# Optimization experiments

Measured on AMD Instinct MI355X. Metric: run time of the kernel, lower is better.

The kernel has to match this reference:

```python
import jax, jax.numpy as jnp
import numpy as np

C = 256
C8 = C // 8
B, H, W = 4, 64, 64


def setup_inputs() -> dict:
    key = jax.random.key(0)
    ks = jax.random.split(key, 10)
    s = lambda fan_in: 1.0 / np.sqrt(fan_in)
    return {
        "x": jax.random.normal(ks[0], (B, C, H, W), dtype=jnp.float32),
        "conv_w": jax.random.normal(ks[1], (C8, C), dtype=jnp.float32) * s(C),
        "conv_b": jax.random.normal(ks[2], (C8,), dtype=jnp.float32) * 0.01,
        "q_w": jax.random.normal(ks[3], (C8, C8), dtype=jnp.float32) * s(C8),
        "q_b": jax.random.normal(ks[4], (C8,), dtype=jnp.float32) * 0.01,
        "k_w": jax.random.normal(ks[5], (C8, C8), dtype=jnp.float32) * s(C8),
        "k_b": jax.random.normal(ks[6], (C8,), dtype=jnp.float32) * 0.01,
        "v_w": jax.random.normal(ks[7], (C, C8), dtype=jnp.float32) * s(C8),
        "v_b": jax.random.normal(ks[8], (C,), dtype=jnp.float32) * 0.01,
        "gamma": jax.random.normal(ks[9], (1,), dtype=jnp.float32) * 0.1,
    }


def reference(x, conv_w, conv_b, q_w, q_b, k_w, k_b, v_w, v_b, gamma):
    b, c, h, w = x.shape
    hw = h * w
    # 1x1 convs are channel-mixing matmuls over flattened spatial dims
    xf = x.reshape(b, c, hw)                                   # [B, C, HW]
    proj = jnp.einsum('dc,bcn->bdn', conv_w, xf) + conv_b[None, :, None]   # [B, C8, HW]
    q = jnp.einsum('ed,bdn->bne', q_w, proj) + q_b[None, None, :]          # [B, HW, C8]
    k = jnp.einsum('ed,bdn->ben', k_w, proj) + k_b[None, :, None]          # [B, C8, HW]
    v = jnp.einsum('cd,bdn->bcn', v_w, proj) + v_b[None, :, None]          # [B, C, HW]
    attn = jax.nn.softmax(jnp.einsum('bne,bem->bnm', q, k), axis=-1)       # [B, HW, HW]
    out = jnp.einsum('bcm,bnm->bcn', v, attn)                              # [B, C, HW]
    out = out.reshape(b, c, h, w)
    return gamma[0] * out + x
```

## Files before the change

### kernel.cpp

```cpp
#include <hip/hip_runtime.h>
#include <hip/hip_bf16.h>
#include <stdint.h>

#define B_   4
#define C_   256
#define C8_  32
#define HW_  4096
#define ROWS_ 320
#define MS_  4
#define L2E  1.4426950408889634f

typedef __attribute__((ext_vector_type(8)))  short  short8;
typedef __attribute__((ext_vector_type(8)))  ushort us8;
typedef __attribute__((ext_vector_type(2)))  float  f32x2;
typedef __attribute__((ext_vector_type(16))) float  f32x16;

#define WT_OFF    0
#define BALL_OFF  (256*320*4)
#define Q_OFF     (BALL_OFF + 1280)
#define KT_OFF    (Q_OFF  + B_*HW_*C8_*2)
#define V_OFF     (KT_OFF + B_*HW_*C8_*2)
#define PACC_OFF  (V_OFF  + B_*C_*HW_*2)
#define LPART_OFF (PACC_OFF + (size_t)MS_*B_*C_*HW_*2)

__device__ __forceinline__ ushort f2bf(float f) {
    union { float f; uint32_t u; } v; v.f = f;
    uint32_t u = v.u;
    uint32_t r = u + 0x7fffu + ((u >> 16) & 1u);
    return (ushort)(r >> 16);
}
__device__ __forceinline__ uint32_t pktr(float lo, float hi) {
    union { float f; uint32_t u; } a, b; a.f = lo; b.f = hi;
    return __builtin_amdgcn_perm(b.u, a.u, 0x07060302u);
}
__device__ __forceinline__ uint32_t pkrne(float lo, float hi) {
    uint32_t r;
    asm("v_cvt_pk_bf16_f32 %0, %1, %2" : "=v"(r) : "v"(lo), "v"(hi));
    return r;
}
__device__ __forceinline__ uint32_t fexp2_pk(float s0, float s1, f32x2& e01) {
    f32x2 s = {s0, s1};
    f32x2 y = __builtin_elementwise_fma(s, (f32x2)(8388608.0f),
                                        (f32x2)(1064992506.0f));
    y = __builtin_elementwise_max(y, (f32x2)(0.0f));
    union { int i; float f; } c0, c1;
    c0.i = (int)y.x;  c1.i = (int)y.y;
    e01.x = c0.f;  e01.y = c1.f;
    return __builtin_amdgcn_perm((uint32_t)c1.i, (uint32_t)c0.i, 0x07060302u);
}

__global__ __launch_bounds__(256) void k_setup(
    const float* __restrict__ conv_w, const float* __restrict__ conv_b,
    const float* __restrict__ q_w, const float* __restrict__ q_b,
    const float* __restrict__ k_w, const float* __restrict__ k_b,
    const float* __restrict__ v_w, const float* __restrict__ v_b,
    ushort* __restrict__ wbf, float* __restrict__ ball)
{
    int r = blockIdx.x;
    int c = threadIdx.x;
    const float* wrow;
    float bias;
    if (r < 32)       { wrow = q_w + r*32;      bias = q_b[r];      }
    else if (r < 64)  { wrow = k_w + (r-32)*32; bias = k_b[r-32];   }
    else              { wrow = v_w + (r-64)*32; bias = v_b[r-64];   }
    float acc = 0.f;
    #pragma unroll
    for (int d = 0; d < 32; ++d) acc += wrow[d] * conv_w[d*C_ + c];
    float scale = (r < 32) ? L2E : 1.0f;
    int lanew = (r & 31) + 32*((c >> 3) & 1);
    int fidx  = (c >> 4)*10 + (r >> 5);
    wbf[fidx*512 + lanew*8 + (c & 7)] = f2bf(acc * scale);
    if (c == 0) {
        float bb = bias;
        #pragma unroll
        for (int d = 0; d < 32; ++d) bb += wrow[d] * conv_b[d];
        ball[r] = bb * scale;
    }
}

__global__ __launch_bounds__(320) void k_qkv(
    const float* __restrict__ x, const ushort* __restrict__ wbf,
    const float* __restrict__ ball,
    ushort* __restrict__ qg, ushort* __restrict__ ktg, ushort* __restrict__ vg)
{
    __shared__ ushort tr[5][32*40];

    int blk = blockIdx.x;
    int b  = blk >> 7;
    int nt = blk & 127;
    int n0 = nt * 32;
    int t = threadIdx.x;
    int w = t >> 6, lane = t & 63;
    int l31 = lane & 31, h = lane >> 5;

    f32x16 acc[2];
    acc[0] = (f32x16)(0.f);
    acc[1] = (f32x16)(0.f);

    const float* xb = x + (size_t)b*C_*HW_ + n0 + l31;

    #pragma unroll 4
    for (int kc = 0; kc < 16; ++kc) {
        short8 a0 = *(const short8*)(wbf + (kc*10 + w*2    )*512 + lane*8);
        short8 a1 = *(const short8*)(wbf + (kc*10 + w*2 + 1)*512 + lane*8);
        const float* xc = xb + (size_t)(kc*16 + h*8)*HW_;
        float xv[8];
        #pragma unroll
        for (int j = 0; j < 8; ++j) xv[j] = xc[(size_t)j*HW_];
        union { uint32_t d[4]; short8 s8; } bf;
        #pragma unroll
        for (int j2 = 0; j2 < 4; ++j2) bf.d[j2] = pktr(xv[2*j2], xv[2*j2+1]);
        acc[0] = __builtin_amdgcn_mfma_f32_32x32x16_bf16(a0, bf.s8, acc[0], 0, 0, 0);
        acc[1] = __builtin_amdgcn_mfma_f32_32x32x16_bf16(a1, bf.s8, acc[1], 0, 0, 0);
    }

    #pragma unroll
    for (int mi = 0; mi < 2; ++mi) {
        int rowb = w*64 + mi*32;
        bool isQK = (rowb < 64);
        float4 bv[4];
        #pragma unroll
        for (int g = 0; g < 4; ++g)
            bv[g] = *(const float4*)(ball + rowb + g*8 + 4*h);
        if (isQK) {
            #pragma unroll
            for (int p = 0; p < 8; ++p) {
                int r0 = 2*p;
                int g  = r0 >> 2;
                int i0 = r0 & 3;
                float f0 = acc[mi][r0]     + ((const float*)&bv[g])[i0];
                float f1 = acc[mi][r0 + 1] + ((const float*)&bv[g])[i0 + 1];
                uint32_t pk = pkrne(f0, f1);
                int roff0 = i0 + 8*g + 4*h;
                *(uint32_t*)(&tr[w][l31*40 + roff0]) = pk;
            }
            #pragma unroll
            for (int f = 0; f < 2; ++f) {
                us8 frag = *(const us8*)(&tr[w][l31*40 + f*16 + h*8]);
                ushort* dstb = (rowb == 0) ? qg : ktg;
                size_t ad = ((size_t)((b*128 + nt)*2 + f) << 9) + lane*8;
                *(us8*)(dstb + ad) = frag;
            }
        } else {
            #pragma unroll
            for (int p = 0; p < 8; ++p) {
                int r0 = 2*p;
                int g  = r0 >> 2;
                int i0 = r0 & 3;
                float f0 = acc[mi][r0]     + ((const float*)&bv[g])[i0];
                float f1 = acc[mi][r0 + 1] + ((const float*)&bv[g])[i0 + 1];
                uint32_t pk = pkrne(f0, f1);
                int roff0 = i0 + 8*g + 4*h;
                tr[w][(roff0    )*40 + l31] = (ushort)pk;
                tr[w][(roff0 + 1)*40 + l31] = (ushort)(pk >> 16);
            }
            #pragma unroll
            for (int f = 0; f < 2; ++f) {
                us8 frag = *(const us8*)(&tr[w][l31*40 + f*16 + h*8]);
                int cblk = (rowb - 64) >> 5;
                int mb = nt*2 + f;
                size_t ad = ((size_t)((b*8 + cblk)*256 + mb) << 9) + lane*8;
                *(us8*)(vg + ad) = frag;
            }
        }
    }
}

__global__ __launch_bounds__(512, 4) void k_attn(
    const ushort* __restrict__ qg, const ushort* __restrict__ ktg,
    const ushort* __restrict__ vg,
    ushort* __restrict__ pacc, float* __restrict__ lpart)
{
    __shared__ ushort v_lds[2][16*512];
    __shared__ ushort kt_lds[2][4*512];

    int blk = blockIdx.x;
    int ms = blk & 3;
    int cs = (blk >> 2) & 1;
    int qb = (blk >> 3) & 15;
    int b  = blk >> 7;
    int t = threadIdx.x;
    int w = t >> 6, lane = t & 63;
    int l31 = lane & 31, h = lane >> 5;
    int mbase = ms*1024;

    short8 qf[2];
    #pragma unroll
    for (int ks = 0; ks < 2; ++ks)
        qf[ks] = *(const short8*)(qg
            + ((size_t)((b*128 + qb*8 + w)*2 + ks) << 9) + lane*8);

    f32x16 acc[4];
    #pragma unroll
    for (int j = 0; j < 4; ++j) acc[j] = (f32x16)(0.f);
    f32x2 lacc0 = {0.f, 0.f};
    f32x2 lacc1 = {0.f, 0.f};

    #define STAGE(buf, m0)                                                          \
    {                                                                               \
        _Pragma("unroll")                                                           \
        for (int ff = 0; ff < 2; ++ff) {                                            \
            int f = w*2 + ff;                                                       \
            int cfr = f >> 2, mf = f & 3;                                           \
            const ushort* src = vg + ((size_t)((b*8 + cs*4 + cfr)*256               \
                                 + ((m0) >> 4) + mf) << 9) + lane*8;                \
            __builtin_amdgcn_global_load_lds(                                       \
                (const __attribute__((address_space(1))) uint32_t*)src,             \
                (__attribute__((address_space(3))) uint32_t*)&v_lds[buf][f*512],    \
                16, 0, 0);                                                          \
        }                                                                           \
        if (w < 4) {                                                                \
            const ushort* src = ktg + ((size_t)((b*128 + ((m0) >> 5) + (w >> 1))*2  \
                                 + (w & 1)) << 9) + lane*8;                         \
            __builtin_amdgcn_global_load_lds(                                       \
                (const __attribute__((address_space(1))) uint32_t*)src,             \
                (__attribute__((address_space(3))) uint32_t*)&kt_lds[buf][w*512],   \
                16, 0, 0);                                                          \
        }                                                                           \
    }

    #define PMERGE(uu, lo8, hi8)                                                    \
    {                                                                               \
        union { uint32_t d[4]; short8 s8; } fe_, fo_;                               \
        auto r02 = __builtin_amdgcn_permlane32_swap((int)uu[0], (int)uu[2], false, false); \
        auto r13 = __builtin_amdgcn_permlane32_swap((int)uu[1], (int)uu[3], false, false); \
        auto r46 = __builtin_amdgcn_permlane32_swap((int)uu[4], (int)uu[6], false, false); \
        auto r57 = __builtin_amdgcn_permlane32_swap((int)uu[5], (int)uu[7], false, false); \
        fe_.d[0] = (uint32_t)r02[0];  fe_.d[1] = (uint32_t)r13[0];                  \
        fe_.d[2] = (uint32_t)r02[1];  fe_.d[3] = (uint32_t)r13[1];                  \
        fo_.d[0] = (uint32_t)r46[0];  fo_.d[1] = (uint32_t)r57[0];                  \
        fo_.d[2] = (uint32_t)r46[1];  fo_.d[3] = (uint32_t)r57[1];                  \
        lo8 = fe_.s8;  hi8 = fo_.s8;                                               \
    }

    STAGE(0, mbase)
    __syncthreads();

    int buf = 0;
    for (int it = 0; it < 16; ++it) {
        if (it + 1 < 16) STAGE(buf ^ 1, mbase + (it+1)*64)

        short8 kt0a = *(const short8*)(&kt_lds[buf][0*512 + lane*8]);
        short8 kt1a = *(const short8*)(&kt_lds[buf][1*512 + lane*8]);
        f32x16 s_a = (f32x16)(0.f);
        __builtin_amdgcn_s_setprio(1);
        s_a = __builtin_amdgcn_mfma_f32_32x32x16_bf16(kt0a, qf[0], s_a, 0, 0, 0);
        s_a = __builtin_amdgcn_mfma_f32_32x32x16_bf16(kt1a, qf[1], s_a, 0, 0, 0);
        __builtin_amdgcn_s_setprio(0);

        uint32_t ua[8];
        #pragma unroll
        for (int i = 0; i < 8; ++i) {
            f32x2 e01;
            ua[i] = fexp2_pk(s_a[2*i], s_a[2*i+1], e01);
            if (i & 1) lacc1 += e01; else lacc0 += e01;
        }
        short8 pfa0, pfa1;
        PMERGE(ua, pfa0, pfa1)

        short8 kt0b = *(const short8*)(&kt_lds[buf][2*512 + lane*8]);
        short8 kt1b = *(const short8*)(&kt_lds[buf][3*512 + lane*8]);
        f32x16 s_b = (f32x16)(0.f);
        s_b = __builtin_amdgcn_mfma_f32_32x32x16_bf16(kt0b, qf[0], s_b, 0, 0, 0);
        s_b = __builtin_amdgcn_mfma_f32_32x32x16_bf16(kt1b, qf[1], s_b, 0, 0, 0);

        uint32_t ub[8];
        #pragma unroll
        for (int i = 0; i < 8; ++i) {
            f32x2 e01;
            ub[i] = fexp2_pk(s_b[2*i], s_b[2*i+1], e01);
            if (i & 1) lacc1 += e01; else lacc0 += e01;
        }
        #pragma unroll
        for (int msub = 0; msub < 2; ++msub) {
            short8 pfm = msub ? pfa1 : pfa0;
            int ks16 = msub;
            #pragma unroll
            for (int cfr = 0; cfr < 4; ++cfr) {
                short8 vf = *(const short8*)(&v_lds[buf][(cfr*4 + ks16)*512 + lane*8]);
                acc[cfr] = __builtin_amdgcn_mfma_f32_32x32x16_bf16(vf, pfm, acc[cfr], 0, 0, 0);
            }
        }
        short8 pfb0, pfb1;
        PMERGE(ub, pfb0, pfb1)

        __builtin_amdgcn_s_setprio(1);
        #pragma unroll
        for (int msub = 0; msub < 2; ++msub) {
            short8 pfm = msub ? pfb1 : pfb0;
            int ks16 = 2 + msub;
            #pragma unroll
            for (int cfr = 0; cfr < 4; ++cfr) {
                short8 vf = *(const short8*)(&v_lds[buf][(cfr*4 + ks16)*512 + lane*8]);
                acc[cfr] = __builtin_amdgcn_mfma_f32_32x32x16_bf16(vf, pfm, acc[cfr], 0, 0, 0);
            }
        }
        __builtin_amdgcn_s_setprio(0);

        __syncthreads();
        buf ^= 1;
    }

    f32x2 lacc = lacc0 + lacc1;
    float lsum = lacc.x + lacc.y;
    {
        union { float f; int i; } cv; cv.f = lsum;
        cv.i = __shfl_xor(cv.i, 32);
        lsum += cv.f;
    }
    if (cs == 0 && h == 0)
        lpart[(size_t)(ms*B_ + b)*HW_ + qb*256 + w*32 + l31] = lsum;

    int blkl = ((ms*B_ + b)*16 + qb)*2 + cs;
    #pragma unroll
    for (int cfr = 0; cfr < 4; ++cfr) {
        union { uint32_t d[8]; us8 hlf[2]; } pk;
        #pragma unroll
        for (int i = 0; i < 8; ++i)
            pk.d[i] = pktr(acc[cfr][2*i], acc[cfr][2*i+1]);
        ushort* dst = pacc + ((size_t)(blkl*32 + w*4 + cfr) << 10);
        *(us8*)(dst + lane*8)       = pk.hlf[0];
        *(us8*)(dst + 512 + lane*8) = pk.hlf[1];
    }
    #undef STAGE
    #undef PMERGE
}

__global__ __launch_bounds__(256) void k_comb(
    const ushort* __restrict__ pacc, const float* __restrict__ lpart,
    const float* __restrict__ x, const float* __restrict__ gamma_p,
    float* __restrict__ out)
{
    __shared__ float lds_acc[128*36];

    int blk = blockIdx.x;
    int w  = blk & 7;
    int cs = (blk >> 3) & 1;
    int qb = (blk >> 4) & 15;
    int b  = blk >> 8;
    int t = threadIdx.x;

    int l31 = t & 31;
    int h   = (t >> 5) & 1;
    int cfr = (t >> 6) & 3;
    int q = qb*256 + w*32 + l31;
    int lanef = h*32 + l31;

    float sum[16];
    #pragma unroll
    for (int k = 0; k < 16; ++k) sum[k] = 0.f;
    float lt = 0.f;

    #pragma unroll
    for (int ms = 0; ms < MS_; ++ms) {
        int blkl = ((ms*B_ + b)*16 + qb)*2 + cs;
        const ushort* pp = pacc + ((size_t)(blkl*32 + w*4 + cfr) << 10) + lanef*8;
        us8 a0 = *(const us8*)pp;
        us8 a1 = *(const us8*)(pp + 512);
        #pragma unroll
        for (int k = 0; k < 8; ++k) {
            union { uint32_t u; float f; } cv;
            cv.u = ((uint32_t)a0[k]) << 16;  sum[k]   += cv.f;
            cv.u = ((uint32_t)a1[k]) << 16;  sum[k+8] += cv.f;
        }
        lt += lpart[(size_t)(ms*B_ + b)*HW_ + q];
    }

    float rl = gamma_p[0] / lt;
    #pragma unroll
    for (int k = 0; k < 16; ++k) {
        int c = cfr*32 + (k & 3) + 8*(k >> 2) + 4*h;
        lds_acc[c*36 + l31] = sum[k]*rl;
    }
    __syncthreads();

    const float* xb = x + ((size_t)(b*C_ + cs*128))*HW_ + qb*256 + w*32;
    float* ob = out + ((size_t)(b*C_ + cs*128))*HW_ + qb*256 + w*32;
    #pragma unroll
    for (int i = 0; i < 4; ++i) {
        int s = t + i*256;
        int c = s >> 3, qg = s & 7;
        float4 a = *(const float4*)(&lds_acc[c*36 + qg*4]);
        size_t off = (size_t)c*HW_ + qg*4;
        float4 xv = *(const float4*)(xb + off);
        a.x += xv.x; a.y += xv.y; a.z += xv.z; a.w += xv.w;
        *(float4*)(ob + off) = a;
    }
}

extern "C" void kernel_launch(void* const* d_in, const int* in_sizes, int n_in,
                              void* d_out, int out_size, void* d_ws, size_t ws_size,
                              hipStream_t stream)
{
    const float* x      = (const float*)d_in[0];
    const float* conv_w = (const float*)d_in[1];
    const float* conv_b = (const float*)d_in[2];
    const float* q_w    = (const float*)d_in[3];
    const float* q_b    = (const float*)d_in[4];
    const float* k_w    = (const float*)d_in[5];
    const float* k_b    = (const float*)d_in[6];
    const float* v_w    = (const float*)d_in[7];
    const float* v_b    = (const float*)d_in[8];
    const float* gamma  = (const float*)d_in[9];
    float* out = (float*)d_out;

    char* ws = (char*)d_ws;
    ushort* wbf   = (ushort*)(ws + WT_OFF);
    float*  ball  = (float*)(ws + BALL_OFF);
    ushort* qg    = (ushort*)(ws + Q_OFF);
    ushort* ktg   = (ushort*)(ws + KT_OFF);
    ushort* vg    = (ushort*)(ws + V_OFF);
    ushort* pacc  = (ushort*)(ws + PACC_OFF);
    float*  lpart = (float*)(ws + LPART_OFF);

    k_setup<<<ROWS_, 256, 0, stream>>>(conv_w, conv_b, q_w, q_b, k_w, k_b,
                                       v_w, v_b, wbf, ball);
    k_qkv<<<B_*128, 320, 0, stream>>>(x, wbf, ball, qg, ktg, vg);
    k_attn<<<512, 512, 0, stream>>>(qg, ktg, vg, pacc, lpart);
    k_comb<<<1024, 256, 0, stream>>>(pacc, lpart, x, gamma, out);
}
```

Measured before the change: 154.3 us.

## Triple-buffer K/V LDS staging with explicit vmcnt waits in attention loop

Grows the V and K^T LDS staging from two buffers to three, so tiles are prefetched two iterations ahead instead of one. Each iteration now begins with a partial s_waitcnt vmcnt that leaves the newest stage in flight, followed by a single raw s_barrier. This replaces the __syncthreads that waited on all outstanding loads at the end of each iteration. The goal is to hide more global-to-LDS latency behind the MFMA and exp work. The cost is 50% more LDS per block, which could limit how many blocks fit on a CU. The correctness of the hand-written vmcnt counts depends on each wave's exact load count.

Measured after the change: 154.8 us. No clear change (+0.4%).

```diff
diff --git a/kernel.cpp b/kernel.cpp
--- a/kernel.cpp
+++ b/kernel.cpp
@@ -171,8 +171,8 @@
     const ushort* __restrict__ vg,
     ushort* __restrict__ pacc, float* __restrict__ lpart)
 {
-    __shared__ ushort v_lds[2][16*512];
-    __shared__ ushort kt_lds[2][4*512];
+    __shared__ ushort v_lds[3][16*512];
+    __shared__ ushort kt_lds[3][4*512];
 
     int blk = blockIdx.x;
     int ms = blk & 3;
@@ -196,7 +196,7 @@
     f32x2 lacc0 = {0.f, 0.f};
     f32x2 lacc1 = {0.f, 0.f};
 
-    #define STAGE(buf, m0)                                                          \
+    #define STAGE(bi, m0)                                                           \
     {                                                                               \
         _Pragma("unroll")                                                           \
         for (int ff = 0; ff < 2; ++ff) {                                            \
@@ -206,7 +206,7 @@
                                  + ((m0) >> 4) + mf) << 9) + lane*8;                \
             __builtin_amdgcn_global_load_lds(                                       \
                 (const __attribute__((address_space(1))) uint32_t*)src,             \
-                (__attribute__((address_space(3))) uint32_t*)&v_lds[buf][f*512],    \
+                (__attribute__((address_space(3))) uint32_t*)&v_lds[bi][f*512],     \
                 16, 0, 0);                                                          \
         }                                                                           \
         if (w < 4) {                                                                \
@@ -214,7 +214,7 @@
                                  + (w & 1)) << 9) + lane*8;                         \
             __builtin_amdgcn_global_load_lds(                                       \
                 (const __attribute__((address_space(1))) uint32_t*)src,             \
-                (__attribute__((address_space(3))) uint32_t*)&kt_lds[buf][w*512],   \
+                (__attribute__((address_space(3))) uint32_t*)&kt_lds[bi][w*512],    \
                 16, 0, 0);                                                          \
         }                                                                           \
     }
@@ -234,14 +234,25 @@
     }
 
     STAGE(0, mbase)
-    __syncthreads();
-
-    int buf = 0;
+    STAGE(1, mbase + 64)
+
+    int b0 = 0, b1 = 1, b2 = 2;
+    #pragma unroll 1
     for (int it = 0; it < 16; ++it) {
-        if (it + 1 < 16) STAGE(buf ^ 1, mbase + (it+1)*64)
-
-        short8 kt0a = *(const short8*)(&kt_lds[buf][0*512 + lane*8]);
-        short8 kt1a = *(const short8*)(&kt_lds[buf][1*512 + lane*8]);
+        if (it == 15)   { asm volatile("s_waitcnt vmcnt(0)" ::: "memory"); }
+        else if (w < 4) { asm volatile("s_waitcnt vmcnt(3)" ::: "memory"); }
+        else            { asm volatile("s_waitcnt vmcnt(2)" ::: "memory"); }
+        __builtin_amdgcn_s_barrier();
+        __builtin_amdgcn_sched_barrier(0);
+
+        if (it + 2 < 16) STAGE(b2, mbase + (it+2)*64)
+        __builtin_amdgcn_sched_barrier(0);
+
+        const ushort* vbuf = &v_lds[b0][0];
+        const ushort* kbuf = &kt_lds[b0][0];
+
+        short8 kt0a = *(const short8*)(kbuf + 0*512 + lane*8);
+        short8 kt1a = *(const short8*)(kbuf + 1*512 + lane*8);
         f32x16 s_a = (f32x16)(0.f);
         __builtin_amdgcn_s_setprio(1);
         s_a = __builtin_amdgcn_mfma_f32_32x32x16_bf16(kt0a, qf[0], s_a, 0, 0, 0);
@@ -258,8 +269,8 @@
         short8 pfa0, pfa1;
         PMERGE(ua, pfa0, pfa1)
 
-        short8 kt0b = *(const short8*)(&kt_lds[buf][2*512 + lane*8]);
-        short8 kt1b = *(const short8*)(&kt_lds[buf][3*512 + lane*8]);
+        short8 kt0b = *(const short8*)(kbuf + 2*512 + lane*8);
+        short8 kt1b = *(const short8*)(kbuf + 3*512 + lane*8);
         f32x16 s_b = (f32x16)(0.f);
         s_b = __builtin_amdgcn_mfma_f32_32x32x16_bf16(kt0b, qf[0], s_b, 0, 0, 0);
         s_b = __builtin_amdgcn_mfma_f32_32x32x16_bf16(kt1b, qf[1], s_b, 0, 0, 0);
@@ -277,7 +288,7 @@
             int ks16 = msub;
             #pragma unroll
             for (int cfr = 0; cfr < 4; ++cfr) {
-                short8 vf = *(const short8*)(&v_lds[buf][(cfr*4 + ks16)*512 + lane*8]);
+                short8 vf = *(const short8*)(vbuf + (cfr*4 + ks16)*512 + lane*8);
                 acc[cfr] = __builtin_amdgcn_mfma_f32_32x32x16_bf16(vf, pfm, acc[cfr], 0, 0, 0);
             }
         }
@@ -291,14 +302,13 @@
             int ks16 = 2 + msub;
             #pragma unroll
             for (int cfr = 0; cfr < 4; ++cfr) {
-                short8 vf = *(const short8*)(&v_lds[buf][(cfr*4 + ks16)*512 + lane*8]);
+                short8 vf = *(const short8*)(vbuf + (cfr*4 + ks16)*512 + lane*8);
                 acc[cfr] = __builtin_amdgcn_mfma_f32_32x32x16_bf16(vf, pfm, acc[cfr], 0, 0, 0);
             }
         }
         __builtin_amdgcn_s_setprio(0);
 
-        __syncthreads();
-        buf ^= 1;
+        int tb = b0; b0 = b1; b1 = b2; b2 = tb;
     }
 
     f32x2 lacc = lacc0 + lacc1;
```

## Fuse four kernels into one persistent kernel with software grid barriers

Applied to the files above, without the earlier changes.

Merges the setup, QKV projection, attention and combine kernels into a single 512-block kernel separated by atomic-counter grid barriers, and adds a memset to reset the barrier counters. The aim is to remove three kernel launch gaps and their tail effects. In exchange, all 512 blocks must be co-resident for the barrier to work, and the QKV phase leaves 192 threads per block idle. Barrier spin cost and reduced occupancy flexibility may offset the launch savings.

New measurement: 344.8 us. +123.5%, slower.

```diff
diff --git a/kernel.cpp b/kernel.cpp
--- a/kernel.cpp
+++ b/kernel.cpp
@@ -8,6 +8,7 @@
 #define HW_  4096
 #define ROWS_ 320
 #define MS_  4
+#define NB_  512
 #define L2E  1.4426950408889634f
 
 typedef __attribute__((ext_vector_type(8)))  short  short8;
@@ -22,6 +23,7 @@
 #define V_OFF     (KT_OFF + B_*HW_*C8_*2)
 #define PACC_OFF  (V_OFF  + B_*C_*HW_*2)
 #define LPART_OFF (PACC_OFF + (size_t)MS_*B_*C_*HW_*2)
+#define GB_OFF    (LPART_OFF + (size_t)MS_*B_*HW_*4)
 
 __device__ __forceinline__ ushort f2bf(float f) {
     union { float f; uint32_t u; } v; v.f = f;
@@ -49,342 +51,375 @@
     return __builtin_amdgcn_perm((uint32_t)c1.i, (uint32_t)c0.i, 0x07060302u);
 }
 
-__global__ __launch_bounds__(256) void k_setup(
+__device__ __forceinline__ void gridbar(uint32_t* cnt, uint32_t* gen) {
+    __syncthreads();
+    if (threadIdx.x == 0) {
+        __threadfence();
+        uint32_t g = __hip_atomic_load(gen, __ATOMIC_RELAXED,
+                                       __HIP_MEMORY_SCOPE_AGENT);
+        uint32_t old = __hip_atomic_fetch_add(cnt, 1u, __ATOMIC_ACQ_REL,
+                                              __HIP_MEMORY_SCOPE_AGENT);
+        if (old == NB_ - 1u) {
+            __hip_atomic_store(cnt, 0u, __ATOMIC_RELAXED,
+                               __HIP_MEMORY_SCOPE_AGENT);
+            __hip_atomic_fetch_add(gen, 1u, __ATOMIC_RELEASE,
+                                   __HIP_MEMORY_SCOPE_AGENT);
+        } else {
+            long tmo = 200000000;
+            while (__hip_atomic_load(gen, __ATOMIC_RELAXED,
+                                     __HIP_MEMORY_SCOPE_AGENT) == g
+                   && --tmo > 0) ;
+        }
+        __threadfence();
+    }
+    __syncthreads();
+}
+
+__global__ __launch_bounds__(512, 4) void k_fused(
+    const float* __restrict__ x,
     const float* __restrict__ conv_w, const float* __restrict__ conv_b,
     const float* __restrict__ q_w, const float* __restrict__ q_b,
     const float* __restrict__ k_w, const float* __restrict__ k_b,
     const float* __restrict__ v_w, const float* __restrict__ v_b,
-    ushort* __restrict__ wbf, float* __restrict__ ball)
+    const float* __restrict__ gamma_p,
+    float* __restrict__ out,
+    ushort* __restrict__ wbf, float* __restrict__ ball,
+    ushort* __restrict__ qg, ushort* __restrict__ ktg, ushort* __restrict__ vg,
+    ushort* __restrict__ pacc, float* __restrict__ lpart,
+    uint32_t* __restrict__ gb)
 {
-    int r = blockIdx.x;
-    int c = threadIdx.x;
-    const float* wrow;
-    float bias;
-    if (r < 32)       { wrow = q_w + r*32;      bias = q_b[r];      }
-    else if (r < 64)  { wrow = k_w + (r-32)*32; bias = k_b[r-32];   }
-    else              { wrow = v_w + (r-64)*32; bias = v_b[r-64];   }
-    float acc = 0.f;
-    #pragma unroll
-    for (int d = 0; d < 32; ++d) acc += wrow[d] * conv_w[d*C_ + c];
-    float scale = (r < 32) ? L2E : 1.0f;
-    int lanew = (r & 31) + 32*((c >> 3) & 1);
-    int fidx  = (c >> 4)*10 + (r >> 5);
-    wbf[fidx*512 + lanew*8 + (c & 7)] = f2bf(acc * scale);
-    if (c == 0) {
-        float bb = bias;
-        #pragma unroll
-        for (int d = 0; d < 32; ++d) bb += wrow[d] * conv_b[d];
-        ball[r] = bb * scale;
+    __shared__ __align__(16) char smem[40960];
+
+    int blk = blockIdx.x;
+    int t = threadIdx.x;
+    uint32_t* gb_cnt = gb;
+    uint32_t* gb_gen = gb + 1;
+
+    if (blk < ROWS_ && t < 256) {
+        int r = blk;
+        int c = t;
+        const float* wrow;
+        float bias;
+        if (r < 32)       { wrow = q_w + r*32;      bias = q_b[r];      }
+        else if (r < 64)  { wrow = k_w + (r-32)*32; bias = k_b[r-32];   }
+        else              { wrow = v_w + (r-64)*32; bias = v_b[r-64];   }
+        float acc = 0.f;
+        #pragma unroll
+        for (int d = 0; d < 32; ++d) acc += wrow[d] * conv_w[d*C_ + c];
+        float scale = (r < 32) ? L2E : 1.0f;
+        int lanew = (r & 31) + 32*((c >> 3) & 1);
+        int fidx  = (c >> 4)*10 + (r >> 5);
+        wbf[fidx*512 + lanew*8 + (c & 7)] = f2bf(acc * scale);
+        if (c == 0) {
+            float bb = bias;
+            #pragma unroll
+            for (int d = 0; d < 32; ++d) bb += wrow[d] * conv_b[d];
+            ball[r] = bb * scale;
+        }
     }
-}
-
-__global__ __launch_bounds__(320) void k_qkv(
-    const float* __restrict__ x, const ushort* __restrict__ wbf,
-    const float* __restrict__ ball,
-    ushort* __restrict__ qg, ushort* __restrict__ ktg, ushort* __restrict__ vg)
-{
-    __shared__ ushort tr[5][32*40];
-
-    int blk = blockIdx.x;
-    int b  = blk >> 7;
-    int nt = blk & 127;
-    int n0 = nt * 32;
-    int t = threadIdx.x;
-    int w = t >> 6, lane = t & 63;
-    int l31 = lane & 31, h = lane >> 5;
-
-    f32x16 acc[2];
-    acc[0] = (f32x16)(0.f);
-    acc[1] = (f32x16)(0.f);
-
-    const float* xb = x + (size_t)b*C_*HW_ + n0 + l31;
-
-    #pragma unroll 4
-    for (int kc = 0; kc < 16; ++kc) {
-        short8 a0 = *(const short8*)(wbf + (kc*10 + w*2    )*512 + lane*8);
-        short8 a1 = *(const short8*)(wbf + (kc*10 + w*2 + 1)*512 + lane*8);
-        const float* xc = xb + (size_t)(kc*16 + h*8)*HW_;
-        float xv[8];
-        #pragma unroll
-        for (int j = 0; j < 8; ++j) xv[j] = xc[(size_t)j*HW_];
-        union { uint32_t d[4]; short8 s8; } bf;
-        #pragma unroll
-        for (int j2 = 0; j2 < 4; ++j2) bf.d[j2] = pktr(xv[2*j2], xv[2*j2+1]);
-        acc[0] = __builtin_amdgcn_mfma_f32_32x32x16_bf16(a0, bf.s8, acc[0], 0, 0, 0);
-        acc[1] = __builtin_amdgcn_mfma_f32_32x32x16_bf16(a1, bf.s8, acc[1], 0, 0, 0);
+    gridbar(gb_cnt, gb_gen);
+
+    if (t < 320) {
+        ushort (*tr)[32*40] = (ushort (*)[32*40])smem;
+
+        int b  = blk >> 7;
+        int nt = blk & 127;
+        int n0 = nt * 32;
+        int w = t >> 6, lane = t & 63;
+        int l31 = lane & 31, h = lane >> 5;
+
+        f32x16 acc[2];
+        acc[0] = (f32x16)(0.f);
+        acc[1] = (f32x16)(0.f);
+
+        const float* xb = x + (size_t)b*C_*HW_ + n0 + l31;
+
+        #pragma unroll 4
+        for (int kc = 0; kc < 16; ++kc) {
+            short8 a0 = *(const short8*)(wbf + (kc*10 + w*2    )*512 + lane*8);
+            short8 a1 = *(const short8*)(wbf + (kc*10 + w*2 + 1)*512 + lane*8);
+            const float* xc = xb + (size_t)(kc*16 + h*8)*HW_;
+            float xv[8];
+            #pragma unroll
+            for (int j = 0; j < 8; ++j) xv[j] = xc[(size_t)j*HW_];
+            union { uint32_t d[4]; short8 s8; } bf;
+            #pragma unroll
+            for (int j2 = 0; j2 < 4; ++j2) bf.d[j2] = pktr(xv[2*j2], xv[2*j2+1]);
+            acc[0] = __builtin_amdgcn_mfma_f32_32x32x16_bf16(a0, bf.s8, acc[0], 0, 0, 0);
+            acc[1] = __builtin_amdgcn_mfma_f32_32x32x16_bf16(a1, bf.s8, acc[1], 0, 0, 0);
+        }
+
+        #pragma unroll
+        for (int mi = 0; mi < 2; ++mi) {
+            int rowb = w*64 + mi*32;
+            bool isQK = (rowb < 64);
+            float4 bv[4];
+            #pragma unroll
+            for (int g = 0; g < 4; ++g)
+                bv[g] = *(const float4*)(ball + rowb + g*8 + 4*h);
+            if (isQK) {
+                #pragma unroll
+                for (int p = 0; p < 8; ++p) {
+                    int r0 = 2*p;
+                    int g  = r0 >> 2;
+                    int i0 = r0 & 3;
+                    float f0 = acc[mi][r0]     + ((const float*)&bv[g])[i0];
+                    float f1 = acc[mi][r0 + 1] + ((const float*)&bv[g])[i0 + 1];
+                    uint32_t pk = pkrne(f0, f1);
+                    int roff0 = i0 + 8*g + 4*h;
+                    *(uint32_t*)(&tr[w][l31*40 + roff0]) = pk;
+                }
+                #pragma unroll
+                for (int f = 0; f < 2; ++f) {
+                    us8 frag = *(const us8*)(&tr[w][l31*40 + f*16 + h*8]);
+                    ushort* dstb = (rowb == 0) ? qg : ktg;
+                    size_t ad = ((size_t)((b*128 + nt)*2 + f) << 9) + lane*8;
+                    *(us8*)(dstb + ad) = frag;
+                }
+            } else {
+                #pragma unroll
+                for (int p = 0; p < 8; ++p) {
+                    int r0 = 2*p;
+                    int g  = r0 >> 2;
+                    int i0 = r0 & 3;
+                    float f0 = acc[mi][r0]     + ((const float*)&bv[g])[i0];
+                    float f1 = acc[mi][r0 + 1] + ((const float*)&bv[g])[i0 + 1];
+                    uint32_t pk = pkrne(f0, f1);
+                    int roff0 = i0 + 8*g + 4*h;
+                    tr[w][(roff0    )*40 + l31] = (ushort)pk;
+                    tr[w][(roff0 + 1)*40 + l31] = (ushort)(pk >> 16);
+                }
+                #pragma unroll
+                for (int f = 0; f < 2; ++f) {
+                    us8 frag = *(const us8*)(&tr[w][l31*40 + f*16 + h*8]);
+                    int cblk = (rowb - 64) >> 5;
+                    int mb = nt*2 + f;
+                    size_t ad = ((size_t)((b*8 + cblk)*256 + mb) << 9) + lane*8;
+                    *(us8*)(vg + ad) = frag;
+                }
+            }
+        }
     }
-
-    #pragma unroll
-    for (int mi = 0; mi < 2; ++mi) {
-        int rowb = w*64 + mi*32;
-        bool isQK = (rowb < 64);
-        float4 bv[4];
-        #pragma unroll
-        for (int g = 0; g < 4; ++g)
-            bv[g] = *(const float4*)(ball + rowb + g*8 + 4*h);
-        if (isQK) {
-            #pragma unroll
-            for (int p = 0; p < 8; ++p) {
-                int r0 = 2*p;
-                int g  = r0 >> 2;
-                int i0 = r0 & 3;
-                float f0 = acc[mi][r0]     + ((const float*)&bv[g])[i0];
-                float f1 = acc[mi][r0 + 1] + ((const float*)&bv[g])[i0 + 1];
-                uint32_t pk = pkrne(f0, f1);
-                int roff0 = i0 + 8*g + 4*h;
-                *(uint32_t*)(&tr[w][l31*40 + roff0]) = pk;
-            }
-            #pragma unroll
-            for (int f = 0; f < 2; ++f) {
-                us8 frag = *(const us8*)(&tr[w][l31*40 + f*16 + h*8]);
-                ushort* dstb = (rowb == 0) ? qg : ktg;
-                size_t ad = ((size_t)((b*128 + nt)*2 + f) << 9) + lane*8;
-                *(us8*)(dstb + ad) = frag;
-            }
-        } else {
-            #pragma unroll
-            for (int p = 0; p < 8; ++p) {
-                int r0 = 2*p;
-                int g  = r0 >> 2;
-                int i0 = r0 & 3;
-                float f0 = acc[mi][r0]     + ((const float*)&bv[g])[i0];
-                float f1 = acc[mi][r0 + 1] + ((const float*)&bv[g])[i0 + 1];
-                uint32_t pk = pkrne(f0, f1);
-                int roff0 = i0 + 8*g + 4*h;
-                tr[w][(roff0    )*40 + l31] = (ushort)pk;
-                tr[w][(roff0 + 1)*40 + l31] = (ushort)(pk >> 16);
-            }
-            #pragma unroll
-            for (int f = 0; f < 2; ++f) {
-                us8 frag = *(const us8*)(&tr[w][l31*40 + f*16 + h*8]);
-                int cblk = (rowb - 64) >> 5;
-                int mb = nt*2 + f;
-                size_t ad = ((size_t)((b*8 + cblk)*256 + mb) << 9) + lane*8;
-                *(us8*)(vg + ad) = frag;
-            }
-        }
+    gridbar(gb_cnt, gb_gen);
+
+    {
+        ushort* v_lds  = (ushort*)smem;
+        ushort* kt_lds = (ushort*)(smem + 32768);
+
+        int ms = blk & 3;
+        int cs = (blk >> 2) & 1;
+        int qb = (blk >> 3) & 15;
+        int b  = blk >> 7;
+        int w = t >> 6, lane = t & 63;
+        int l31 = lane & 31, h = lane >> 5;
+        int mbase = ms*1024;
+
+        short8 qf[2];
+        #pragma unroll
+        for (int ks = 0; ks < 2; ++ks)
+            qf[ks] = *(const short8*)(qg
+                + ((size_t)((b*128 + qb*8 + w)*2 + ks) << 9) + lane*8);
+
+        f32x16 acc[4];
+        #pragma unroll
+        for (int j = 0; j < 4; ++j) acc[j] = (f32x16)(0.f);
+        f32x2 lacc0 = {0.f, 0.f};
+        f32x2 lacc1 = {0.f, 0.f};
+
+        #define STAGE(bi, m0)                                                          \
+        {                                                                              \
+            _Pragma("unroll")                                                          \
+            for (int ff = 0; ff < 2; ++ff) {                                           \
+                int f = w*2 + ff;                                                      \
+                int cfr = f >> 2, mf = f & 3;                                          \
+                const ushort* src = vg + ((size_t)((b*8 + cs*4 + cfr)*256              \
+                                     + ((m0) >> 4) + mf) << 9) + lane*8;               \
+                __builtin_amdgcn_global_load_lds(                                      \
+                    (const __attribute__((address_space(1))) uint32_t*)src,            \
+                    (__attribute__((address_space(3))) uint32_t*)                      \
+                        &v_lds[(bi)*8192 + f*512],                                     \
+                    16, 0, 0);                                                         \
+            }                                                                          \
+            if (w < 4) {                                                               \
+                const ushort* src = ktg + ((size_t)((b*128 + ((m0) >> 5) + (w >> 1))*2 \
+                                     + (w & 1)) << 9) + lane*8;                        \
+                __builtin_amdgcn_global_load_lds(                                      \
+                    (const __attribute__((address_space(1))) uint32_t*)src,            \
+                    (__attribute__((address_space(3))) uint32_t*)                      \
+                        &kt_lds[(bi)*2048 + w*512],                                    \
+                    16, 0, 0);                                                         \
+            }                                                                          \
+        }
+
+        #define PMERGE(uu, lo8, hi8)                                                   \
+        {                                                                              \
+            union { uint32_t d[4]; short8 s8; } fe_, fo_;                              \
+            auto r02 = __builtin_amdgcn_permlane32_swap((int)uu[0], (int)uu[2], false, false); \
+            auto r13 = __builtin_amdgcn_permlane32_swap((int)uu[1], (int)uu[3], false, false); \
+            auto r46 = __builtin_amdgcn_permlane32_swap((int)uu[4], (int)uu[6], false, false); \
+            auto r57 = __builtin_amdgcn_permlane32_swap((int)uu[5], (int)uu[7], false, false); \
+            fe_.d[0] = (uint32_t)r02[0];  fe_.d[1] = (uint32_t)r13[0];                 \
+            fe_.d[2] = (uint32_t)r02[1];  fe_.d[3] = (uint32_t)r13[1];                 \
+            fo_.d[0] = (uint32_t)r46[0];  fo_.d[1] = (uint32_t)r57[0];                 \
+            fo_.d[2] = (uint32_t)r46[1];  fo_.d[3] = (uint32_t)r57[1];                 \
+            lo8 = fe_.s8;  hi8 = fo_.s8;                                              \
+        }
+
+        STAGE(0, mbase)
+        __syncthreads();
+
+        int buf = 0;
+        for (int it = 0; it < 16; ++it) {
+            if (it + 1 < 16) STAGE(buf ^ 1, mbase + (it+1)*64)
+
+            const ushort* vbuf = &v_lds[buf*8192];
+            const ushort* kbuf = &kt_lds[buf*2048];
+
+            short8 kt0a = *(const short8*)(kbuf + 0*512 + lane*8);
+            short8 kt1a = *(const short8*)(kbuf + 1*512 + lane*8);
+            f32x16 s_a = (f32x16)(0.f);
+            __builtin_amdgcn_s_setprio(1);
+            s_a = __builtin_amdgcn_mfma_f32_32x32x16_bf16(kt0a, qf[0], s_a, 0, 0, 0);
+            s_a = __builtin_amdgcn_mfma_f32_32x32x16_bf16(kt1a, qf[1], s_a, 0, 0, 0);
+            __builtin_amdgcn_s_setprio(0);
+
+            uint32_t ua[8];
+            #pragma unroll
+            for (int i = 0; i < 8; ++i) {
+                f32x2 e01;
+                ua[i] = fexp2_pk(s_a[2*i], s_a[2*i+1], e01);
+                if (i & 1) lacc1 += e01; else lacc0 += e01;
+            }
+            short8 pfa0, pfa1;
+            PMERGE(ua, pfa0, pfa1)
+
+            short8 kt0b = *(const short8*)(kbuf + 2*512 + lane*8);
+            short8 kt1b = *(const short8*)(kbuf + 3*512 + lane*8);
+            f32x16 s_b = (f32x16)(0.f);
+            s_b = __builtin_amdgcn_mfma_f32_32x32x16_bf16(kt0b, qf[0], s_b, 0, 0, 0);
+            s_b = __builtin_amdgcn_mfma_f32_32x32x16_bf16(kt1b, qf[1], s_b, 0, 0, 0);
+
+            uint32_t ub[8];
+            #pragma unroll
+            for (int i = 0; i < 8; ++i) {
+                f32x2 e01;
+                ub[i] = fexp2_pk(s_b[2*i], s_b[2*i+1], e01);
+                if (i & 1) lacc1 += e01; else lacc0 += e01;
+            }
+            #pragma unroll
+            for (int msub = 0; msub < 2; ++msub) {
+                short8 pfm = msub ? pfa1 : pfa0;
+                int ks16 = msub;
+                #pragma unroll
+                for (int cfr = 0; cfr < 4; ++cfr) {
+                    short8 vf = *(const short8*)(vbuf + (cfr*4 + ks16)*512 + lane*8);
+                    acc[cfr] = __builtin_amdgcn_mfma_f32_32x32x16_bf16(vf, pfm, acc[cfr], 0, 0, 0);
+                }
+            }
+            short8 pfb0, pfb1;
+            PMERGE(ub, pfb0, pfb1)
+
+            __builtin_amdgcn_s_setprio(1);
+            #pragma unroll
+            for (int msub = 0; msub < 2; ++msub) {
+                short8 pfm = msub ? pfb1 : pfb0;
+                int ks16 = 2 + msub;
+                #pragma unroll
+                for (int cfr = 0; cfr < 4; ++cfr) {
+                    short8 vf = *(const short8*)(vbuf + (cfr*4 + ks16)*512 + lane*8);
+                    acc[cfr] = __builtin_amdgcn_mfma_f32_32x32x16_bf16(vf, pfm, acc[cfr], 0, 0, 0);
+                }
+            }
+            __builtin_amdgcn_s_setprio(0);
+
+            __syncthreads();
+            buf ^= 1;
+        }
+
+        f32x2 lacc = lacc0 + lacc1;
+        float lsum = lacc.x + lacc.y;
+        {
+            union { float f; int i; } cv; cv.f = lsum;
+            cv.i = __shfl_xor(cv.i, 32);
+            lsum += cv.f;
+        }
+        if (cs == 0 && h == 0)
+            lpart[(size_t)(ms*B_ + b)*HW_ + qb*256 + w*32 + l31] = lsum;
+
+        int blkl = ((ms*B_ + b)*16 + qb)*2 + cs;
+        #pragma unroll
+        for (int cfr = 0; cfr < 4; ++cfr) {
+            union { uint32_t d[8]; us8 hlf[2]; } pk;
+            #pragma unroll
+            for (int i = 0; i < 8; ++i)
+                pk.d[i] = pktr(acc[cfr][2*i], acc[cfr][2*i+1]);
+            ushort* dst = pacc + ((size_t)(blkl*32 + w*4 + cfr) << 10);
+            *(us8*)(dst + lane*8)       = pk.hlf[0];
+            *(us8*)(dst + 512 + lane*8) = pk.hlf[1];
+        }
+        #undef STAGE
+        #undef PMERGE
     }
-}
-
-__global__ __launch_bounds__(512, 4) void k_attn(
-    const ushort* __restrict__ qg, const ushort* __restrict__ ktg,
-    const ushort* __restrict__ vg,
-    ushort* __restrict__ pacc, float* __restrict__ lpart)
-{
-    __shared__ ushort v_lds[2][16*512];
-    __shared__ ushort kt_lds[2][4*512];
-
-    int blk = blockIdx.x;
-    int ms = blk & 3;
-    int cs = (blk >> 2) & 1;
-    int qb = (blk >> 3) & 15;
-    int b  = blk >> 7;
-    int t = threadIdx.x;
-    int w = t >> 6, lane = t & 63;
-    int l31 = lane & 31, h = lane >> 5;
-    int mbase = ms*1024;
-
-    short8 qf[2];
-    #pragma unroll
-    for (int ks = 0; ks < 2; ++ks)
-        qf[ks] = *(const short8*)(qg
-            + ((size_t)((b*128 + qb*8 + w)*2 + ks) << 9) + lane*8);
-
-    f32x16 acc[4];
-    #pragma unroll
-    for (int j = 0; j < 4; ++j) acc[j] = (f32x16)(0.f);
-    f32x2 lacc0 = {0.f, 0.f};
-    f32x2 lacc1 = {0.f, 0.f};
-
-    #define STAGE(buf, m0)                                                          \
-    {                                                                               \
-        _Pragma("unroll")                                                           \
-        for (int ff = 0; ff < 2; ++ff) {                                            \
-            int f = w*2 + ff;                                                       \
-            int cfr = f >> 2, mf = f & 3;                                           \
-            const ushort* src = vg + ((size_t)((b*8 + cs*4 + cfr)*256               \
-                                 + ((m0) >> 4) + mf) << 9) + lane*8;                \
-            __builtin_amdgcn_global_load_lds(                                       \
-                (const __attribute__((address_space(1))) uint32_t*)src,             \
-                (__attribute__((address_space(3))) uint32_t*)&v_lds[buf][f*512],    \
-                16, 0, 0);                                                          \
-        }                                                                           \
-        if (w < 4) {                                                                \
-            const ushort* src = ktg + ((size_t)((b*128 + ((m0) >> 5) + (w >> 1))*2  \
-                                 + (w & 1)) << 9) + lane*8;                         \
-            __builtin_amdgcn_global_load_lds(                                       \
-                (const __attribute__((address_space(1))) uint32_t*)src,             \
-                (__attribute__((address_space(3))) uint32_t*)&kt_lds[buf][w*512],   \
-                16, 0, 0);                                                          \
-        }                                                                           \
-    }
-
-    #define PMERGE(uu, lo8, hi8)                                                    \
-    {                                                                               \
-        union { uint32_t d[4]; short8 s8; } fe_, fo_;                               \
-        auto r02 = __builtin_amdgcn_permlane32_swap((int)uu[0], (int)uu[2], false, false); \
-        auto r13 = __builtin_amdgcn_permlane32_swap((int)uu[1], (int)uu[3], false, false); \
-        auto r46 = __builtin_amdgcn_permlane32_swap((int)uu[4], (int)uu[6], false, false); \
-        auto r57 = __builtin_amdgcn_permlane32_swap((int)uu[5], (int)uu[7], false, false); \
-        fe_.d[0] = (uint32_t)r02[0];  fe_.d[1] = (uint32_t)r13[0];                  \
-        fe_.d[2] = (uint32_t)r02[1];  fe_.d[3] = (uint32_t)r13[1];                  \
-        fo_.d[0] = (uint32_t)r46[0];  fo_.d[1] = (uint32_t)r57[0];                  \
-        fo_.d[2] = (uint32_t)r46[1];  fo_.d[3] = (uint32_t)r57[1];                  \
-        lo8 = fe_.s8;  hi8 = fo_.s8;                                               \
-    }
-
-    STAGE(0, mbase)
-    __syncthreads();
-
-    int buf = 0;
-    for (int it = 0; it < 16; ++it) {
-        if (it + 1 < 16) STAGE(buf ^ 1, mbase + (it+1)*64)
-
-        short8 kt0a = *(const short8*)(&kt_lds[buf][0*512 + lane*8]);
-        short8 kt1a = *(const short8*)(&kt_lds[buf][1*512 + lane*8]);
-        f32x16 s_a = (f32x16)(0.f);
-        __builtin_amdgcn_s_setprio(1);
-        s_a = __builtin_amdgcn_mfma_f32_32x32x16_bf16(kt0a, qf[0], s_a, 0, 0, 0);
-        s_a = __builtin_amdgcn_mfma_f32_32x32x16_bf16(kt1a, qf[1], s_a, 0, 0, 0);
-        __builtin_amdgcn_s_setprio(0);
-
-        uint32_t ua[8];
-        #pragma unroll
-        for (int i = 0; i < 8; ++i) {
-            f32x2 e01;
-            ua[i] = fexp2_pk(s_a[2*i], s_a[2*i+1], e01);
-            if (i & 1) lacc1 += e01; else lacc0 += e01;
-        }
-        short8 pfa0, pfa1;
-        PMERGE(ua, pfa0, pfa1)
-
-        short8 kt0b = *(const short8*)(&kt_lds[buf][2*512 + lane*8]);
-        short8 kt1b = *(const short8*)(&kt_lds[buf][3*512 + lane*8]);
-        f32x16 s_b = (f32x16)(0.f);
-        s_b = __builtin_amdgcn_mfma_f32_32x32x16_bf16(kt0b, qf[0], s_b, 0, 0, 0);
-        s_b = __builtin_amdgcn_mfma_f32_32x32x16_bf16(kt1b, qf[1], s_b, 0, 0, 0);
-
-        uint32_t ub[8];
-        #pragma unroll
-        for (int i = 0; i < 8; ++i) {
-            f32x2 e01;
-            ub[i] = fexp2_pk(s_b[2*i], s_b[2*i+1], e01);
-            if (i & 1) lacc1 += e01; else lacc0 += e01;
-        }
-        #pragma unroll
-        for (int msub = 0; msub < 2; ++msub) {
-            short8 pfm = msub ? pfa1 : pfa0;
-            int ks16 = msub;
-            #pragma unroll
-            for (int cfr = 0; cfr < 4; ++cfr) {
-                short8 vf = *(const short8*)(&v_lds[buf][(cfr*4 + ks16)*512 + lane*8]);
-                acc[cfr] = __builtin_amdgcn_mfma_f32_32x32x16_bf16(vf, pfm, acc[cfr], 0, 0, 0);
-            }
-        }
-        short8 pfb0, pfb1;
-        PMERGE(ub, pfb0, pfb1)
-
-        __builtin_amdgcn_s_setprio(1);
-        #pragma unroll
-        for (int msub = 0; msub < 2; ++msub) {
-            short8 pfm = msub ? pfb1 : pfb0;
-            int ks16 = 2 + msub;
-            #pragma unroll
-            for (int cfr = 0; cfr < 4; ++cfr) {
-                short8 vf = *(const short8*)(&v_lds[buf][(cfr*4 + ks16)*512 + lane*8]);
-                acc[cfr] = __builtin_amdgcn_mfma_f32_32x32x16_bf16(vf, pfm, acc[cfr], 0, 0, 0);
-            }
-        }
-        __builtin_amdgcn_s_setprio(0);
-
+    gridbar(gb_cnt, gb_gen);
+
+    {
+        int half = t >> 8;
+        int tl = t & 255;
+        int vb = blk*2 + half;
+
+        int w3  = vb & 7;
+        int cs3 = (vb >> 3) & 1;
+        int qb3 = (vb >> 4) & 15;
+        int b3  = vb >> 8;
+
+        float* lds_acc = (float*)(smem + half*18432);
+
+        int l31 = tl & 31;
+        int h3  = (tl >> 5) & 1;
+        int cfr = (tl >> 6) & 3;
+        int q = qb3*256 + w3*32 + l31;
+        int lanef = h3*32 + l31;
+
+        float sum[16];
+        #pragma unroll
+        for (int k = 0; k < 16; ++k) sum[k] = 0.f;
+        float lt = 0.f;
+
+        #pragma unroll
+        for (int ms = 0; ms < MS_; ++ms) {
+            int blkl = ((ms*B_ + b3)*16 + qb3)*2 + cs3;
+            const ushort* pp = pacc + ((size_t)(blkl*32 + w3*4 + cfr) << 10) + lanef*8;
+            us8 a0 = *(const us8*)pp;
+            us8 a1 = *(const us8*)(pp + 512);
+            #pragma unroll
+            for (int k = 0; k < 8; ++k) {
+                union { uint32_t u; float f; } cv;
+                cv.u = ((uint32_t)a0[k]) << 16;  sum[k]   += cv.f;
+                cv.u = ((uint32_t)a1[k]) << 16;  sum[k+8] += cv.f;
+            }
+            lt += lpart[(size_t)(ms*B_ + b3)*HW_ + q];
+        }
+
+        float rl = gamma_p[0] / lt;
+        #pragma unroll
+        for (int k = 0; k < 16; ++k) {
+            int c = cfr*32 + (k & 3) + 8*(k >> 2) + 4*h3;
+            lds_acc[c*36 + l31] = sum[k]*rl;
+        }
         __syncthreads();
-        buf ^= 1;
-    }
-
-    f32x2 lacc = lacc0 + lacc1;
-    float lsum = lacc.x + lacc.y;
-    {
-        union { float f; int i; } cv; cv.f = lsum;
-        cv.i = __shfl_xor(cv.i, 32);
-        lsum += cv.f;
-    }
-    if (cs == 0 && h == 0)
-        lpart[(size_t)(ms*B_ + b)*HW_ + qb*256 + w*32 + l31] = lsum;
-
-    int blkl = ((ms*B_ + b)*16 + qb)*2 + cs;
-    #pragma unroll
-    for (int cfr = 0; cfr < 4; ++cfr) {
-        union { uint32_t d[8]; us8 hlf[2]; } pk;
-        #pragma unroll
-        for (int i = 0; i < 8; ++i)
-            pk.d[i] = pktr(acc[cfr][2*i], acc[cfr][2*i+1]);
-        ushort* dst = pacc + ((size_t)(blkl*32 + w*4 + cfr) << 10);
-        *(us8*)(dst + lane*8)       = pk.hlf[0];
-        *(us8*)(dst + 512 + lane*8) = pk.hlf[1];
-    }
-    #undef STAGE
-    #undef PMERGE
-}
-
-__global__ __launch_bounds__(256) void k_comb(
-    const ushort* __restrict__ pacc, const float* __restrict__ lpart,
-    const float* __restrict__ x, const float* __restrict__ gamma_p,
-    float* __restrict__ out)
-{
-    __shared__ float lds_acc[128*36];
-
-    int blk = blockIdx.x;
-    int w  = blk & 7;
-    int cs = (blk >> 3) & 1;
-    int qb = (blk >> 4) & 15;
-    int b  = blk >> 8;
-    int t = threadIdx.x;
-
-    int l31 = t & 31;
-    int h   = (t >> 5) & 1;
-    int cfr = (t >> 6) & 3;
-    int q = qb*256 + w*32 + l31;
-    int lanef = h*32 + l31;
-
-    float sum[16];
-    #pragma unroll
-    for (int k = 0; k < 16; ++k) sum[k] = 0.f;
-    float lt = 0.f;
-
-    #pragma unroll
-    for (int ms = 0; ms < MS_; ++ms) {
-        int blkl = ((ms*B_ + b)*16 + qb)*2 + cs;
-        const ushort* pp = pacc + ((size_t)(blkl*32 + w*4 + cfr) << 10) + lanef*8;
-        us8 a0 = *(const us8*)pp;
-        us8 a1 = *(const us8*)(pp + 512);
-        #pragma unroll
-        for (int k = 0; k < 8; ++k) {
-            union { uint32_t u; float f; } cv;
-            cv.u = ((uint32_t)a0[k]) << 16;  sum[k]   += cv.f;
-            cv.u = ((uint32_t)a1[k]) << 16;  sum[k+8] += cv.f;
-        }
-        lt += lpart[(size_t)(ms*B_ + b)*HW_ + q];
-    }
-
-    float rl = gamma_p[0] / lt;
-    #pragma unroll
-    for (int k = 0; k < 16; ++k) {
-        int c = cfr*32 + (k & 3) + 8*(k >> 2) + 4*h;
-        lds_acc[c*36 + l31] = sum[k]*rl;
-    }
-    __syncthreads();
-
-    const float* xb = x + ((size_t)(b*C_ + cs*128))*HW_ + qb*256 + w*32;
-    float* ob = out + ((size_t)(b*C_ + cs*128))*HW_ + qb*256 + w*32;
-    #pragma unroll
-    for (int i = 0; i < 4; ++i) {
-        int s = t + i*256;
-        int c = s >> 3, qg = s & 7;
-        float4 a = *(const float4*)(&lds_acc[c*36 + qg*4]);
-        size_t off = (size_t)c*HW_ + qg*4;
-        float4 xv = *(const float4*)(xb + off);
-        a.x += xv.x; a.y += xv.y; a.z += xv.z; a.w += xv.w;
-        *(float4*)(ob + off) = a;
+
+        const float* xb = x + ((size_t)(b3*C_ + cs3*128))*HW_ + qb3*256 + w3*32;
+        float* ob = out + ((size_t)(b3*C_ + cs3*128))*HW_ + qb3*256 + w3*32;
+        #pragma unroll
+        for (int i = 0; i < 4; ++i) {
+            int s = tl + i*256;
+            int c = s >> 3, qg2 = s & 7;
+            float4 a = *(const float4*)(&lds_acc[c*36 + qg2*4]);
+            size_t off = (size_t)c*HW_ + qg2*4;
+            float4 xv = *(const float4*)(xb + off);
+            a.x += xv.x; a.y += xv.y; a.z += xv.z; a.w += xv.w;
+            *(float4*)(ob + off) = a;
+        }
     }
 }
 
@@ -412,10 +447,11 @@
     ushort* vg    = (ushort*)(ws + V_OFF);
     ushort* pacc  = (ushort*)(ws + PACC_OFF);
     float*  lpart = (float*)(ws + LPART_OFF);
-
-    k_setup<<<ROWS_, 256, 0, stream>>>(conv_w, conv_b, q_w, q_b, k_w, k_b,
-                                       v_w, v_b, wbf, ball);
-    k_qkv<<<B_*128, 320, 0, stream>>>(x, wbf, ball, qg, ktg, vg);
-    k_attn<<<512, 512, 0, stream>>>(qg, ktg, vg, pacc, lpart);
-    k_comb<<<1024, 256, 0, stream>>>(pacc, lpart, x, gamma, out);
-}
+    uint32_t* gb  = (uint32_t*)(ws + GB_OFF);
+
+    hipMemsetAsync(gb, 0, 64, stream);
+
+    k_fused<<<NB_, 512, 0, stream>>>(
+        x, conv_w, conv_b, q_w, q_b, k_w, k_b, v_w, v_b, gamma, out,
+        wbf, ball, qg, ktg, vg, pacc, lpart, gb);
+}
```
